# Performance work log

Hardware: AMD Instinct MI355X
Metric: run time of the kernel (lower is better)

## Reference

```python
import jax, jax.numpy as jnp
import numpy as np

N, IN_F, OUT_F, H = 4096, 256, 512, 8
D = OUT_F // H  # hidden per head
NEG_SLOPE = 0.2


def setup_inputs() -> dict:
    key = jax.random.key(0)
    k1, k2, k3 = jax.random.split(key, 3)
    inp = jax.random.normal(k1, (N, IN_F), dtype=jnp.float32)
    A = jnp.zeros((N, N), dtype=jnp.float32)  # additive adjacency mask
    # xavier_uniform for W [out, in]
    limW = float(np.sqrt(6.0 / (IN_F + H * D)))
    W = jax.random.uniform(k2, (H * D, IN_F), minval=-limW, maxval=limW, dtype=jnp.float32)
    lima = float(np.sqrt(6.0 / (H * D + 1)))
    a_left = jax.random.uniform(k3, (1, H, D), minval=-lima, maxval=lima, dtype=jnp.float32)
    return {"inp": inp, "A": A, "W": W, "a_left": a_left}


def reference(inp, A, W, a_left):
    # h: [N, H, D]
    h = (inp @ W.T).reshape(-1, H, D)
    # NOTE: source uses a_left for BOTH source and target scores (a_right is dead code)
    scores = jnp.sum(h * a_left, axis=-1)  # [N, H]
    s = scores.T  # [H, N]
    # [H, N, N] additive attention logits
    logits = jax.nn.leaky_relu(s[:, :, None] + s[:, None, :], negative_slope=NEG_SLOPE)
    logits = logits + A[None, :, :]
    att = jax.nn.softmax(logits, axis=-1)  # [H, N, N]
    # bmm: [H,N,N] x [H,N,D] -> [H,N,D] -> [N,H,D]
    out = jnp.einsum('hij,jhd->ihd', att, h)
    return out.reshape(-1, H * D)
```

## Files before the change

### kernel.cpp

```cpp
#include <hip/hip_runtime.h>
#include <hip/hip_bf16.h>
#include <math.h>

#define N 4096
#define IN_F 256
#define OUT_F 512
#define H 8
#define D 64
#define NEG 0.2f
#define LOG2E 1.44269504f

typedef __attribute__((ext_vector_type(8))) short bf16x8;
typedef __attribute__((ext_vector_type(4))) float f32x4;

__device__ __forceinline__ float leaky(float x) { return fmaxf(x, NEG * x); }

__device__ __forceinline__ unsigned short f2bf(float x) {
    union { float f; unsigned u; } v; v.f = x;
    unsigned r = v.u + 0x7fff + ((v.u >> 16) & 1);
    return (unsigned short)(r >> 16);
}

__device__ __forceinline__ unsigned pk_bf16(float a, float b) {
    __hip_bfloat162 h2 = __float22bfloat162_rn(float2{a, b});
    union { __hip_bfloat162 h; unsigned u; } u; u.h = h2;
    return u.u;
}

__device__ __forceinline__ unsigned fmap(float x) {
    union { float f; unsigned u; } v; v.f = x;
    return (v.u & 0x80000000u) ? ~v.u : (v.u | 0x80000000u);
}
__device__ __forceinline__ float funmap(unsigned m) {
    union { float f; unsigned u; } v;
    v.u = (m & 0x80000000u) ? (m & 0x7fffffffu) : ~m;
    return v.f;
}

__device__ __forceinline__ void dma16(const void* g, void* l) {
    __builtin_amdgcn_global_load_lds((const __attribute__((address_space(1))) void*)g,
                                     (__attribute__((address_space(3))) void*)l, 16, 0, 0);
}

__global__ __launch_bounds__(256) void k_gemm(const float* __restrict__ inp,
                                              const float* __restrict__ W,
                                              const float* __restrict__ a_left,
                                              unsigned short* __restrict__ hbT,
                                              float* __restrict__ s,
                                              unsigned* __restrict__ smaxU) {
    __shared__ float As[64][69];
    __shared__ float Bs[64][69];
    __shared__ unsigned short h_st[64][72];
    __shared__ float s_red[64];

    const int t = threadIdx.x;
    const int bi = blockIdx.x;
    const int head = blockIdx.y;
    const int ty = t >> 4, tx = t & 15;
    const int lr = t >> 2;
    const int cq = (t & 3) * 16;

    float4 pa[4], pb[4];
    auto loadrk = [&](int k0) {
        const float* ip = &inp[(size_t)(bi * 64 + lr) * IN_F + k0 + cq];
        const float* wp = &W[(size_t)(head * 64 + lr) * IN_F + k0 + cq];
#pragma unroll
        for (int q = 0; q < 4; ++q) {
            pa[q] = *(const float4*)&ip[q * 4];
            pb[q] = *(const float4*)&wp[q * 4];
        }
    };
    loadrk(0);

    float acc[4][4] = {};
    for (int k0 = 0; k0 < IN_F; k0 += 64) {
        __syncthreads();
#pragma unroll
        for (int q = 0; q < 4; ++q)
#pragma unroll
            for (int j = 0; j < 4; ++j) {
                As[cq + q * 4 + j][lr] = ((const float*)&pa[q])[j];
                Bs[cq + q * 4 + j][lr] = ((const float*)&pb[q])[j];
            }
        __syncthreads();
        if (k0 + 64 < IN_F) loadrk(k0 + 64);
#pragma unroll
        for (int k = 0; k < 64; ++k) {
            float4 a4 = *(const float4*)&As[k][ty * 4];
            float4 b4 = *(const float4*)&Bs[k][tx * 4];
            float a[4] = {a4.x, a4.y, a4.z, a4.w};
            float b[4] = {b4.x, b4.y, b4.z, b4.w};
#pragma unroll
            for (int r = 0; r < 4; ++r)
#pragma unroll
                for (int c = 0; c < 4; ++c) acc[r][c] = fmaf(a[r], b[c], acc[r][c]);
        }
    }

    float aL[4];
#pragma unroll
    for (int c = 0; c < 4; ++c) aL[c] = a_left[head * D + tx * 4 + c];
#pragma unroll
    for (int r = 0; r < 4; ++r) {
        float sp = acc[r][0] * aL[0] + acc[r][1] * aL[1] + acc[r][2] * aL[2] + acc[r][3] * aL[3];
        sp += __shfl_xor(sp, 1); sp += __shfl_xor(sp, 2);
        sp += __shfl_xor(sp, 4); sp += __shfl_xor(sp, 8);
        if (tx == 0) {
            s[head * N + bi * 64 + ty * 4 + r] = sp;
            s_red[ty * 4 + r] = sp;
        }
    }
    __syncthreads();
    if (t < 64) {
        float m = s_red[t];
        for (int off = 32; off; off >>= 1) m = fmaxf(m, __shfl_down(m, off, 64));
        if (t == 0) atomicMax(&smaxU[head], fmap(m));
    }

#pragma unroll
    for (int r = 0; r < 4; ++r) {
        ushort4 v;
        v.x = f2bf(acc[r][0]); v.y = f2bf(acc[r][1]);
        v.z = f2bf(acc[r][2]); v.w = f2bf(acc[r][3]);
        *(ushort4*)&h_st[ty * 4 + r][tx * 4] = v;
    }
    __syncthreads();
    {
        const int d = t >> 2, iq = (t & 3) * 16;
        unsigned short us[16];
#pragma unroll
        for (int k = 0; k < 16; ++k) us[k] = h_st[iq + k][d];
        unsigned short* dst = &hbT[((size_t)(head * D + d)) * N + bi * 64 + iq];
#pragma unroll
        for (int q = 0; q < 4; ++q) {
            ushort4 v = {us[q * 4 + 0], us[q * 4 + 1], us[q * 4 + 2], us[q * 4 + 3]};
            *(ushort4*)&dst[q * 4] = v;
        }
    }
}

__global__ __launch_bounds__(256) void k_rowmax(const float* __restrict__ A,
                                                float* __restrict__ rmax) {
    int i = blockIdx.x;
    const float* row = &A[(size_t)i * N];
    float m = -1e30f;
    for (int j = threadIdx.x * 4; j < N; j += 256 * 4) {
        float4 v = *(const float4*)&row[j];
        m = fmaxf(fmaxf(fmaxf(m, v.x), fmaxf(v.y, v.z)), v.w);
    }
    for (int off = 32; off; off >>= 1) m = fmaxf(m, __shfl_down(m, off, 64));
    __shared__ float red[4];
    if ((threadIdx.x & 63) == 0) red[threadIdx.x >> 6] = m;
    __syncthreads();
    if (threadIdx.x == 0) rmax[i] = fmaxf(fmaxf(red[0], red[1]), fmaxf(red[2], red[3]));
}

__global__ __launch_bounds__(512, 4) void k_attn(const float* __restrict__ A,
                                                 const unsigned short* __restrict__ hbT,
                                                 const float* __restrict__ s,
                                                 const unsigned* __restrict__ smaxU,
                                                 const float* __restrict__ rmax,
                                                 float* __restrict__ out) {
    __shared__ unsigned short hT_st[2][16384];

    const int t = threadIdx.x;
    const int bid = blockIdx.x;
    const int hg = bid & 1;
    const int i0 = (bid >> 1) * 16;

    const int lane = t & 63, wave = t >> 6;
    const int quad = lane >> 4, li = lane & 15;
    const int wh = wave & 3, jh = wave >> 2;
    const int head = hg * 4 + wh;
    const int row = i0 + li;
    const int jb = jh * 2048;
    const int NSTEP = 2048 / 32;
    const int wbase = wave * 2048;

    const float sr = s[head * N + row];
    const float sI = sr * LOG2E;
    const float mb = (leaky(sr + funmap(smaxU[head])) + rmax[row]) * LOG2E;

    const unsigned short* gH[4];
#pragma unroll
    for (int q = 0; q < 4; ++q) {
        int m = q * 64 + lane, Rloc = m >> 2, sl = m & 3;
        int grow = head * 64 + Rloc;
        int jcol = jb + ((sl ^ ((Rloc >> 1) & 3)) * 8);
        gH[q] = &hbT[(size_t)grow * N + jcol];
    }

    const float* Ap = &A[(size_t)row * N + jb + quad * 8];
    const float* sp = &s[(size_t)head * N + jb + quad * 8];

    f32x4 acc[4] = {{0,0,0,0},{0,0,0,0},{0,0,0,0},{0,0,0,0}};
    f32x4 acc_z = {0, 0, 0, 0};
    bf16x8 vones;
#pragma unroll
    for (int k = 0; k < 8; ++k) vones[k] = (short)0x3F80;

    const int hsw = quad ^ ((li >> 1) & 3);

    auto issue_tile = [&](int buf, int jn) {
#pragma unroll
        for (int q = 0; q < 4; ++q)
            dma16(gH[q] + jn, &hT_st[buf][wbase + (q * 64 + lane) * 8]);
    };

    auto compute_tile = [&](int buf, float4 A0, float4 A1, float4 S0, float4 S1) {
        float av[8] = {A0.x, A0.y, A0.z, A0.w, A1.x, A1.y, A1.z, A1.w};
        float sv[8] = {S0.x, S0.y, S0.z, S0.w, S1.x, S1.y, S1.z, S1.w};
        union { bf16x8 v; unsigned u[4]; } P;
#pragma unroll
        for (int p = 0; p < 4; ++p) {
            float x0 = fmaf(sv[2 * p + 0], LOG2E, sI);
            float x1 = fmaf(sv[2 * p + 1], LOG2E, sI);
            float w0 = __builtin_amdgcn_exp2f(fmaxf(x0, NEG * x0) + fmaf(av[2 * p + 0], LOG2E, -mb));
            float w1 = __builtin_amdgcn_exp2f(fmaxf(x1, NEG * x1) + fmaf(av[2 * p + 1], LOG2E, -mb));
            P.u[p] = pk_bf16(w0, w1);
        }
        acc_z = __builtin_amdgcn_mfma_f32_16x16x32_bf16(P.v, vones, acc_z, 0, 0, 0);
        const unsigned short* bH = &hT_st[buf][wbase];
#pragma unroll
        for (int db = 0; db < 4; ++db) {
            const int d = db * 16 + li;
            bf16x8 hf = *(const bf16x8*)&bH[(d * 4 + hsw) * 8];
            acc[db] = __builtin_amdgcn_mfma_f32_16x16x32_bf16(P.v, hf, acc[db], 0, 0, 0);
        }
    };

    issue_tile(0, 0);
    float4 eA0 = *(const float4*)&Ap[0], eA1 = *(const float4*)&Ap[4];
    float4 eS0 = *(const float4*)&sp[0], eS1 = *(const float4*)&sp[4];
    issue_tile(1, 32);
    float4 oA0 = *(const float4*)&Ap[32], oA1 = *(const float4*)&Ap[36];
    float4 oS0 = *(const float4*)&sp[32], oS1 = *(const float4*)&sp[36];

#pragma unroll 1
    for (int itp = 0; itp < NSTEP / 2; ++itp) {
        asm volatile("s_waitcnt vmcnt(8)" ::: "memory");
        __builtin_amdgcn_sched_barrier(0);
        compute_tile(0, eA0, eA1, eS0, eS1);
        if (itp < NSTEP / 2 - 1) {
            const int jn = (2 * itp + 2) * 32;
            issue_tile(0, jn);
            eA0 = *(const float4*)&Ap[jn]; eA1 = *(const float4*)&Ap[jn + 4];
            eS0 = *(const float4*)&sp[jn]; eS1 = *(const float4*)&sp[jn + 4];
        }
        if (itp < NSTEP / 2 - 1) {
            asm volatile("s_waitcnt vmcnt(8)" ::: "memory");
        } else {
            asm volatile("s_waitcnt vmcnt(0)" ::: "memory");
        }
        __builtin_amdgcn_sched_barrier(0);
        compute_tile(1, oA0, oA1, oS0, oS1);
        if (itp < NSTEP / 2 - 1) {
            const int jn = (2 * itp + 3) * 32;
            issue_tile(1, jn);
            oA0 = *(const float4*)&Ap[jn]; oA1 = *(const float4*)&Ap[jn + 4];
            oS0 = *(const float4*)&sp[jn]; oS1 = *(const float4*)&sp[jn + 4];
        }
    }

    __syncthreads();
    float* red = (float*)&hT_st[0][0];
    if (jh == 1) {
        const int base = (wh * 64 + lane) * 21;
#pragma unroll
        for (int db = 0; db < 4; ++db)
#pragma unroll
            for (int r = 0; r < 4; ++r) red[base + db * 4 + r] = acc[db][r];
#pragma unroll
        for (int r = 0; r < 4; ++r) red[base + 16 + r] = acc_z[r];
    }
    __syncthreads();
    if (jh == 0) {
        const int base = (wh * 64 + lane) * 21;
#pragma unroll
        for (int db = 0; db < 4; ++db)
#pragma unroll
            for (int r = 0; r < 4; ++r) acc[db][r] += red[base + db * 4 + r];
#pragma unroll
        for (int r = 0; r < 4; ++r) {
            const float zT = acc_z[r] + red[base + 16 + r];
            const float inv = 1.0f / zT;
            float* op = &out[(size_t)(i0 + quad * 4 + r) * OUT_F + head * D];
#pragma unroll
            for (int db = 0; db < 4; ++db) op[db * 16 + li] = acc[db][r] * inv;
        }
    }
}

extern "C" void kernel_launch(void* const* d_in, const int* in_sizes, int n_in,
                              void* d_out, int out_size, void* d_ws, size_t ws_size,
                              hipStream_t stream) {
    const float* inp = (const float*)d_in[0];
    const float* A = (const float*)d_in[1];
    const float* W = (const float*)d_in[2];
    const float* a_left = (const float*)d_in[3];
    float* out = (float*)d_out;

    unsigned short* hbT = (unsigned short*)d_ws;
    float* s = (float*)((char*)d_ws + (size_t)H * D * N * 2);
    unsigned* smaxU = (unsigned*)(s + (size_t)H * N);
    float* rmax = (float*)(smaxU + 8);

    hipMemsetAsync(smaxU, 0, 8 * sizeof(unsigned), stream);

    k_gemm<<<dim3(N / 64, H), 256, 0, stream>>>(inp, W, a_left, hbT, s, smaxU);
    k_rowmax<<<dim3(N), 256, 0, stream>>>(A, rmax);
    k_attn<<<dim3((N / 16) * 2), 512, 0, stream>>>(A, hbT, s, smaxU, rmax, out);
}
```

Measured before the change: 245.7 us.

## Deepen prefetch pipeline: issue next tile DMA and A/s loads two steps ahead

Restructures the main loop as four-way unrolled, with four register sets for the A-mask and score vectors. Each step now issues the LDS DMA for the next tile and the A/s global loads two tiles ahead before computing the current tile. The old loop issued them after computing. The goal is to hide global-load latency more fully behind the exp and MFMA work, at the cost of more VGPRs, which may reduce occupancy.

Measured after the change: 244.7 us. Within noise of the previous version (-0.4%).

```diff
diff --git a/kernel.cpp b/kernel.cpp
--- a/kernel.cpp
+++ b/kernel.cpp
@@ -207,6 +207,15 @@
             dma16(gH[q] + jn, &hT_st[buf][wbase + (q * 64 + lane) * 8]);
     };
 
+    float4 rA0[4], rA1[4], rS0[4], rS1[4];
+#define LOAD_AS(SET, JN)                                                   \
+    do {                                                                   \
+        rA0[SET] = *(const float4*)&Ap[(JN)];                              \
+        rA1[SET] = *(const float4*)&Ap[(JN) + 4];                          \
+        rS0[SET] = *(const float4*)&sp[(JN)];                              \
+        rS1[SET] = *(const float4*)&sp[(JN) + 4];                          \
+    } while (0)
+
     auto compute_tile = [&](int buf, float4 A0, float4 A1, float4 S0, float4 S1) {
         float av[8] = {A0.x, A0.y, A0.z, A0.w, A1.x, A1.y, A1.z, A1.w};
         float sv[8] = {S0.x, S0.y, S0.z, S0.w, S1.x, S1.y, S1.z, S1.w};
@@ -230,37 +239,34 @@
     };
 
     issue_tile(0, 0);
-    float4 eA0 = *(const float4*)&Ap[0], eA1 = *(const float4*)&Ap[4];
-    float4 eS0 = *(const float4*)&sp[0], eS1 = *(const float4*)&sp[4];
-    issue_tile(1, 32);
-    float4 oA0 = *(const float4*)&Ap[32], oA1 = *(const float4*)&Ap[36];
-    float4 oS0 = *(const float4*)&sp[32], oS1 = *(const float4*)&sp[36];
+    LOAD_AS(0, 0);
+    LOAD_AS(1, 32);
 
 #pragma unroll 1
-    for (int itp = 0; itp < NSTEP / 2; ++itp) {
-        asm volatile("s_waitcnt vmcnt(8)" ::: "memory");
-        __builtin_amdgcn_sched_barrier(0);
-        compute_tile(0, eA0, eA1, eS0, eS1);
-        if (itp < NSTEP / 2 - 1) {
-            const int jn = (2 * itp + 2) * 32;
-            issue_tile(0, jn);
-            eA0 = *(const float4*)&Ap[jn]; eA1 = *(const float4*)&Ap[jn + 4];
-            eS0 = *(const float4*)&sp[jn]; eS1 = *(const float4*)&sp[jn + 4];
-        }
-        if (itp < NSTEP / 2 - 1) {
-            asm volatile("s_waitcnt vmcnt(8)" ::: "memory");
-        } else {
-            asm volatile("s_waitcnt vmcnt(0)" ::: "memory");
-        }
-        __builtin_amdgcn_sched_barrier(0);
-        compute_tile(1, oA0, oA1, oS0, oS1);
-        if (itp < NSTEP / 2 - 1) {
-            const int jn = (2 * itp + 3) * 32;
-            issue_tile(1, jn);
-            oA0 = *(const float4*)&Ap[jn]; oA1 = *(const float4*)&Ap[jn + 4];
-            oS0 = *(const float4*)&sp[jn]; oS1 = *(const float4*)&sp[jn + 4];
-        }
-    }
+    for (int itp = 0; itp < NSTEP / 4; ++itp) {
+#pragma unroll
+        for (int u = 0; u < 4; ++u) {
+            const int t4 = itp * 4 + u;
+            if (t4 + 1 < NSTEP) issue_tile((u + 1) & 1, (t4 + 1) * 32);
+            if (t4 + 2 < NSTEP) {
+                const int jn = (t4 + 2) * 32;
+                switch ((u + 2) & 3) {
+                    case 0: LOAD_AS(0, jn); break;
+                    case 1: LOAD_AS(1, jn); break;
+                    case 2: LOAD_AS(2, jn); break;
+                    case 3: LOAD_AS(3, jn); break;
+                }
+            }
+            if (t4 == NSTEP - 1) {
+                asm volatile("s_waitcnt vmcnt(0)" ::: "memory");
+            } else {
+                asm volatile("s_waitcnt vmcnt(8)" ::: "memory");
+            }
+            __builtin_amdgcn_sched_barrier(0);
+            compute_tile(u & 1, rA0[u], rA1[u], rS0[u], rS1[u]);
+        }
+    }
+#undef LOAD_AS
 
     __syncthreads();
     float* red = (float*)&hT_st[0][0];
```
